# Kernel optimization log

Measured on AMD Instinct MI355X. Metric: run time of the kernel, lower is better.

Reference implementation:

```python
import jax, jax.numpy as jnp
import numpy as np

B, S, D, H = 2, 2048, 1024, 16
HD = D // H  # head_dim = 64


def setup_inputs() -> dict:
    key = jax.random.key(0)
    ks = jax.random.split(key, 6)
    scale = D ** -0.5
    x = jax.random.normal(ks[0], (B, S, D), dtype=jnp.float32)
    wq = jax.random.normal(ks[1], (D, D), dtype=jnp.float32) * scale
    wk = jax.random.normal(ks[2], (D, D), dtype=jnp.float32) * scale
    wv = jax.random.normal(ks[3], (D, D), dtype=jnp.float32) * scale
    wo = jax.random.normal(ks[4], (D, D), dtype=jnp.float32) * scale
    # RoPE frequencies: theta_i = 10000^(-2i/HD), angles[t, i] = t * theta_i
    inv_freq = 1.0 / (10000.0 ** (np.arange(0, HD, 2, dtype=np.float32) / HD))
    t = np.arange(S, dtype=np.float32)
    angles = np.outer(t, inv_freq)  # [S, HD//2]
    freqs_cos = jnp.asarray(np.cos(angles), dtype=jnp.float32)
    freqs_sin = jnp.asarray(np.sin(angles), dtype=jnp.float32)
    # additive causal mask [1,1,S,S]
    neg = jnp.float32(-1e9)
    mask = jnp.triu(jnp.full((S, S), neg, dtype=jnp.float32), k=1)[None, None]
    return {"x": x, "wq": wq, "wk": wk, "wv": wv, "wo": wo,
            "freqs_cos": freqs_cos, "freqs_sin": freqs_sin,
            "mask": mask, "start_pos": 0}


def _apply_rope(q, freqs_cos, freqs_sin):
    # q: [B, S, H, HD] -> pairs (even, odd) rotated by angle per position
    b, s, h, hd = q.shape
    q2 = q.reshape(b, s, h, hd // 2, 2)
    qr, qi = q2[..., 0], q2[..., 1]
    c = freqs_cos[None, :, None, :]  # [1, S, 1, HD//2]
    sn = freqs_sin[None, :, None, :]
    out_r = qr * c - qi * sn
    out_i = qr * sn + qi * c
    return jnp.stack([out_r, out_i], axis=-1).reshape(b, s, h, hd)


def reference(x, wq, wk, wv, wo, freqs_cos, freqs_sin, mask, start_pos):
    b, s, _ = x.shape
    xq = (x @ wq).reshape(b, s, H, HD)
    xk = (x @ wk).reshape(b, s, H, HD)
    xv = (x @ wv).reshape(b, s, H, HD)
    xq = _apply_rope(xq, freqs_cos, freqs_sin)
    xk = _apply_rope(xk, freqs_cos, freqs_sin)
    # [B, H, S, HD]
    q = xq.transpose(0, 2, 1, 3)
    k = xk.transpose(0, 2, 1, 3)
    v = xv.transpose(0, 2, 1, 3)
    scores = jnp.einsum('bhqd,bhkd->bhqk', q, k) / jnp.sqrt(jnp.float32(HD))
    scores = scores + mask
    probs = jax.nn.softmax(scores.astype(jnp.float32), axis=-1).astype(q.dtype)
    out = jnp.einsum('bhqk,bhkd->bhqd', probs, v)
    out = out.transpose(0, 2, 1, 3).reshape(b, s, H * HD)
    return out @ wo
```

## Files before the change

### kernel.cpp

```cpp
#include <hip/hip_runtime.h>

typedef unsigned short u16;
typedef __bf16 bf16x8 __attribute__((ext_vector_type(8)));
typedef float f32x4 __attribute__((ext_vector_type(4)));

#define DD 1024
#define SS 2048
#define HH 16
#define HDIM 64

#define VMCNT(N) asm volatile("s_waitcnt vmcnt(" #N ")" ::: "memory")
#define LGKMCNT0 asm volatile("s_waitcnt lgkmcnt(0)" ::: "memory")
#define MEMFENCE asm volatile("" ::: "memory")
#define SBAR __builtin_amdgcn_s_barrier()

__device__ __forceinline__ u16 f2bf(float f) {
  union { float f; unsigned u; } x; x.f = f;
  unsigned r = x.u + 0x7FFFu + ((x.u >> 16) & 1u);
  return (u16)(r >> 16);
}

__device__ __forceinline__ u16 f2bf_s(float f) {
  unsigned r;
  asm("v_cvt_pk_bf16_f32 %0, %1, %2" : "=v"(r) : "v"(f), "v"(0.f));
  return (u16)r;
}

__device__ __forceinline__ void gload_lds16(const u16* g, u16* l) {
  __builtin_amdgcn_global_load_lds((const __attribute__((address_space(1))) void*)g,
                                   (__attribute__((address_space(3))) void*)l, 16, 0, 0);
}

__global__ __launch_bounds__(256) void prep(const float* __restrict__ x,
                                            const float* __restrict__ w0, const float* __restrict__ w1,
                                            const float* __restrict__ w2, const float* __restrict__ w3,
                                            u16* __restrict__ xb, u16* __restrict__ wT) {
  __shared__ float t[32][33];
  const int id = blockIdx.x;
  const int tid = threadIdx.x;
  if (id < 4096) {
    int i = (id * 256 + tid) * 4;
    float4 v = *(const float4*)(x + i);
    union { u16 u[4]; short4 s4; } pk;
    pk.u[0] = f2bf(v.x);
    pk.u[1] = f2bf(v.y);
    pk.u[2] = f2bf(v.z);
    pk.u[3] = f2bf(v.w);
    *(short4*)(xb + i) = pk.s4;
    return;
  }
  const int tt = id - 4096;
  const int z = tt >> 10;
  const int xy = tt & 1023;
  const int j0 = (xy & 31) * 32;
  const int i0 = (xy >> 5) * 32;
  const float* w = (z == 0) ? w0 : (z == 1) ? w1 : (z == 2) ? w2 : w3;
  u16* o = wT + (size_t)z * DD * DD;
  const int tx = tid & 31, ty = tid >> 5;
#pragma unroll
  for (int r = ty; r < 32; r += 8)
    t[r][tx] = w[(size_t)(i0 + r) * DD + j0 + tx];
  __syncthreads();
#pragma unroll
  for (int r = ty; r < 32; r += 8)
    o[(size_t)(j0 + r) * DD + i0 + tx] = f2bf(t[tx][r]);
}

__global__ __launch_bounds__(512, 4) void gemm_qkv(const u16* __restrict__ xb, const u16* __restrict__ wT,
                                                   const float* __restrict__ fc, const float* __restrict__ fs,
                                                   u16* __restrict__ Qr, u16* __restrict__ Kr, u16* __restrict__ Vt) {
  __shared__ u16 As[2][128 * 64];
  __shared__ u16 Bs[2][192 * 64];
  const int tid = threadIdx.x;
  const int lane = tid & 63, wid = tid >> 6;
  const int wm = wid >> 2, wn = wid & 3;
  const int lr = lane & 15, lg = lane >> 4;
  const int id = blockIdx.x;
  const int wg = (id & 7) * 64 + (id >> 3);
  const int m0 = (wg & 31) * 128, n0 = (wg >> 5) * 192;

  f32x4 acc[4][3];
#pragma unroll
  for (int i = 0; i < 4; ++i)
#pragma unroll
    for (int j = 0; j < 3; ++j) acc[i][j] = (f32x4){0.f, 0.f, 0.f, 0.f};

  auto stage = [&](int buf, int k0) {
#pragma unroll
    for (int i = 0; i < 2; ++i) {
      int c = tid + i * 512;
      int row = c >> 3, j = (c & 7) ^ (row & 7);
      gload_lds16(xb + (size_t)(m0 + row) * DD + k0 + j * 8, &As[buf][c * 8]);
    }
#pragma unroll
    for (int i = 0; i < 3; ++i) {
      int c = tid + i * 512;
      int row = c >> 3, j = (c & 7) ^ (row & 7);
      gload_lds16(wT + (size_t)(n0 + row) * DD + k0 + j * 8, &Bs[buf][c * 8]);
    }
  };

  stage(0, 0);
  for (int kt = 0; kt < 16; ++kt) {
    const int cur = kt & 1;
    LGKMCNT0; SBAR;
    if (kt < 15) {
      stage(cur ^ 1, (kt + 1) * 64);
      VMCNT(5);
    } else {
      VMCNT(0);
    }
    SBAR; MEMFENCE;
#pragma unroll
    for (int ks = 0; ks < 2; ++ks) {
      bf16x8 af[4], bfr[3];
#pragma unroll
      for (int mi = 0; mi < 4; ++mi) {
        int row = wm * 64 + mi * 16 + lr;
        int ch = (ks * 4 + lg) ^ (row & 7);
        af[mi] = *(const bf16x8*)(&As[cur][row * 64 + ch * 8]);
      }
#pragma unroll
      for (int ni = 0; ni < 3; ++ni) {
        int row = wn * 48 + ni * 16 + lr;
        int ch = (ks * 4 + lg) ^ (row & 7);
        bfr[ni] = *(const bf16x8*)(&Bs[cur][row * 64 + ch * 8]);
      }
      __builtin_amdgcn_s_setprio(1);
#pragma unroll
      for (int mi = 0; mi < 4; ++mi)
#pragma unroll
        for (int ni = 0; ni < 3; ++ni)
          acc[mi][ni] = __builtin_amdgcn_mfma_f32_16x16x32_bf16(af[mi], bfr[ni], acc[mi][ni], 0, 0, 0);
      __builtin_amdgcn_s_setprio(0);
    }
  }

#pragma unroll
  for (int mi = 0; mi < 4; ++mi)
#pragma unroll
    for (int ni = 0; ni < 3; ++ni) {
      const int nb = n0 + wn * 48 + ni * 16;
      const int z = nb >> 10;
      const int nn = (nb & 1023) + lr;
      const int h = nn >> 6, hd = nn & 63;
      const int mb = m0 + wm * 64 + mi * 16 + lg * 4;
      const int b = mb >> 11, s = mb & 2047;
      if (z == 2) {
        union { u16 u[4]; short4 v4; } pk;
#pragma unroll
        for (int j = 0; j < 4; ++j) pk.u[j] = f2bf(acc[mi][ni][j]);
        *(short4*)(Vt + ((size_t)(b * HH + h) * HDIM + hd) * SS + s) = pk.v4;
      } else {
        u16* dst = (z == 0) ? Qr : Kr;
#pragma unroll
        for (int j = 0; j < 4; ++j) {
          float v = acc[mi][ni][j];
          float pv = __shfl_xor(v, 1);
          int fi = (s + j) * 32 + (hd >> 1);
          float c = fc[fi], sn = fs[fi];
          float o = ((hd & 1) == 0) ? (v * c - pv * sn) : (pv * sn + v * c);
          dst[((size_t)(b * HH + h) * SS + s + j) * HDIM + hd] = f2bf(o);
        }
      }
    }
}

__device__ __forceinline__ void stage_tile(const u16* __restrict__ Kh, const u16* __restrict__ Vh,
                                           int i2, u16* Kbuf, u16* Vbuf, int tid) {
#pragma unroll
  for (int k = 0; k < 2; ++k) {
    const int c = tid + k * 512;
    const int tt = c >> 9, cl = c & 511;
    const int row = cl >> 3, j = (cl & 7) ^ (row & 7);
    gload_lds16(Kh + (size_t)(i2 * 128 + tt * 64 + row) * HDIM + j * 8, Kbuf + c * 8);
    gload_lds16(Vh + (size_t)row * SS + i2 * 128 + tt * 64 + j * 8, Vbuf + c * 8);
  }
}

__device__ __forceinline__ void attn_pass(int qt, int bh, const u16* __restrict__ Qh,
                                          const u16* __restrict__ Kh, const u16* __restrict__ Vh,
                                          u16* __restrict__ Ob, u16* KbR, u16* VbR, u16* Pw,
                                          int gid, int wq) {
  const int tid = threadIdx.x;
  const int lane = tid & 63;
  const int lr = lane & 15, lg = lane >> 4;
  const int q0 = qt * 64 + wq * 16;

  bf16x8 aq[2];
#pragma unroll
  for (int ks = 0; ks < 2; ++ks)
    aq[ks] = *(const bf16x8*)(Qh + (q0 + lr) * HDIM + ks * 32 + lg * 8);

  bf16x8 ones;
  {
    union { u16 u[8]; bf16x8 v; } ou;
#pragma unroll
    for (int i = 0; i < 8; ++i) ou.u[i] = 0x3F80;
    ones = ou.v;
  }

  f32x4 o[4];
#pragma unroll
  for (int d = 0; d < 4; ++d) o[d] = (f32x4){0.f, 0.f, 0.f, 0.f};
  f32x4 ls = (f32x4){0.f, 0.f, 0.f, 0.f};

  const int n2 = (qt + 2) >> 1;

  __syncthreads();
  stage_tile(Kh, Vh, 0, KbR, VbR, tid);

  for (int i = 0; i < n2; ++i) {
    const int cur = i & 1;
    LGKMCNT0; SBAR;
    if (i + 1 < n2) {
      stage_tile(Kh, Vh, i + 1, KbR + (cur ^ 1) * 8192, VbR + (cur ^ 1) * 8192, tid);
      VMCNT(4);
    } else {
      VMCNT(0);
    }
    SBAR; MEMFENCE;

    const int t = 2 * i + gid;
    const u16* Kt = KbR + cur * 8192 + gid * 4096;
    const u16* Vtl = VbR + cur * 8192 + gid * 4096;

    f32x4 sc[4];
#pragma unroll
    for (int kb = 0; kb < 4; ++kb) sc[kb] = (f32x4){0.f, 0.f, 0.f, 0.f};
    __builtin_amdgcn_s_setprio(1);
#pragma unroll
    for (int ks = 0; ks < 2; ++ks)
#pragma unroll
      for (int kb = 0; kb < 4; ++kb) {
        int row = kb * 16 + lr;
        int ch = (ks * 4 + lg) ^ (row & 7);
        bf16x8 bk = *(const bf16x8*)(Kt + row * 64 + ch * 8);
        sc[kb] = __builtin_amdgcn_mfma_f32_16x16x32_bf16(aq[ks], bk, sc[kb], 0, 0, 0);
      }
    __builtin_amdgcn_s_setprio(0);

    if (t >= qt) {
#pragma unroll
      for (int kb = 0; kb < 4; ++kb)
#pragma unroll
        for (int j = 0; j < 4; ++j) {
          int q = q0 + lg * 4 + j;
          int kk = t * 64 + kb * 16 + lr;
          float e = __expf(sc[kb][j] * 0.125f);
          sc[kb][j] = (kk > q) ? 0.f : e;
        }
    } else {
#pragma unroll
      for (int kb = 0; kb < 4; ++kb)
#pragma unroll
        for (int j = 0; j < 4; ++j)
          sc[kb][j] = __expf(sc[kb][j] * 0.125f);
    }

#pragma unroll
    for (int kb = 0; kb < 4; ++kb)
#pragma unroll
      for (int j = 0; j < 4; ++j) {
        int rr = lg * 4 + j;
        int ccol = kb * 16 + lr;
        int ch = (ccol >> 3) ^ (rr & 7);
        Pw[rr * 64 + ch * 8 + (ccol & 7)] = f2bf_s(sc[kb][j]);
      }
#pragma unroll
    for (int ks = 0; ks < 2; ++ks) {
      int chp = (ks * 4 + lg) ^ (lr & 7);
      bf16x8 ap = *(const bf16x8*)(Pw + lr * 64 + chp * 8);
      __builtin_amdgcn_s_setprio(1);
      ls = __builtin_amdgcn_mfma_f32_16x16x32_bf16(ap, ones, ls, 0, 0, 0);
#pragma unroll
      for (int d = 0; d < 4; ++d) {
        int row = d * 16 + lr;
        int ch = (ks * 4 + lg) ^ (row & 7);
        bf16x8 bv = *(const bf16x8*)(Vtl + row * 64 + ch * 8);
        o[d] = __builtin_amdgcn_mfma_f32_16x16x32_bf16(ap, bv, o[d], 0, 0, 0);
      }
      __builtin_amdgcn_s_setprio(0);
    }
  }

  __syncthreads();
  float* mo = (float*)KbR;
  float* ml = (float*)VbR;
  if (gid == 1) {
#pragma unroll
    for (int d = 0; d < 4; ++d)
#pragma unroll
      for (int j = 0; j < 4; ++j)
        mo[(wq * 16 + lg * 4 + j) * 64 + d * 16 + lr] = o[d][j];
    if (lr == 0) {
#pragma unroll
      for (int j = 0; j < 4; ++j) ml[wq * 16 + lg * 4 + j] = ls[j];
    }
  }
  __syncthreads();
  if (gid == 0) {
    const int b = bh >> 4, h = bh & 15;
#pragma unroll
    for (int d = 0; d < 4; ++d)
#pragma unroll
      for (int j = 0; j < 4; ++j) {
        float val = o[d][j] + mo[(wq * 16 + lg * 4 + j) * 64 + d * 16 + lr];
        float lss = ls[j] + ml[wq * 16 + lg * 4 + j];
        int s = q0 + lg * 4 + j;
        int col = h * HDIM + d * 16 + lr;
        Ob[((size_t)b * SS + s) * DD + col] = f2bf(val / lss);
      }
  }
}

__global__ __launch_bounds__(512, 4) void attn(const u16* __restrict__ Qr, const u16* __restrict__ Kr,
                                               const u16* __restrict__ Vt, u16* __restrict__ Ob) {
  __shared__ u16 Kb[2][2][64 * 64];
  __shared__ u16 Vb[2][2][64 * 64];
  __shared__ u16 Ps[8][16 * 64];
  const int id = blockIdx.x;
  const int xcd = id & 7;
  const int r = id >> 3;
  const int pair = r & 15;
  const int bh = xcd * 4 + (r >> 4);
  const u16* Qh = Qr + (size_t)bh * SS * HDIM;
  const u16* Kh = Kr + (size_t)bh * SS * HDIM;
  const u16* Vh = Vt + (size_t)bh * HDIM * SS;
  const int wid = threadIdx.x >> 6;
  const int gid = wid >> 2, wq = wid & 3;
  u16* Pw = &Ps[wid][0];
  attn_pass(pair, bh, Qh, Kh, Vh, Ob, &Kb[0][0][0], &Vb[0][0][0], Pw, gid, wq);
  attn_pass(31 - pair, bh, Qh, Kh, Vh, Ob, &Kb[0][0][0], &Vb[0][0][0], Pw, gid, wq);
}

__global__ __launch_bounds__(512, 4) void gemm_wo(const u16* __restrict__ Ab, const u16* __restrict__ woT,
                                                  float* __restrict__ out) {
  __shared__ u16 As[2][128 * 64];
  __shared__ u16 Bs[2][128 * 64];
  const int tid = threadIdx.x;
  const int lane = tid & 63, wid = tid >> 6;
  const int wm = wid >> 1, wn = wid & 1;
  const int lr = lane & 15, lg = lane >> 4;
  const int id = blockIdx.x;
  const int wg = (id & 7) * 32 + (id >> 3);
  const int m0 = (wg & 31) * 128, n0 = (wg >> 5) * 128;

  f32x4 acc[2][4];
#pragma unroll
  for (int i = 0; i < 2; ++i)
#pragma unroll
    for (int j = 0; j < 4; ++j) acc[i][j] = (f32x4){0.f, 0.f, 0.f, 0.f};

  auto stage = [&](int buf, int k0) {
#pragma unroll
    for (int i = 0; i < 2; ++i) {
      int c = tid + i * 512;
      int row = c >> 3, j = (c & 7) ^ (row & 7);
      gload_lds16(Ab + (size_t)(m0 + row) * DD + k0 + j * 8, &As[buf][c * 8]);
      gload_lds16(woT + (size_t)(n0 + row) * DD + k0 + j * 8, &Bs[buf][c * 8]);
    }
  };

  stage(0, 0);
  for (int kt = 0; kt < 16; ++kt) {
    const int cur = kt & 1;
    LGKMCNT0; SBAR;
    if (kt < 15) {
      stage(cur ^ 1, (kt + 1) * 64);
      VMCNT(4);
    } else {
      VMCNT(0);
    }
    SBAR; MEMFENCE;
#pragma unroll
    for (int ks = 0; ks < 2; ++ks) {
      bf16x8 af[2], bfr[4];
#pragma unroll
      for (int mi = 0; mi < 2; ++mi) {
        int row = wm * 32 + mi * 16 + lr;
        int ch = (ks * 4 + lg) ^ (row & 7);
        af[mi] = *(const bf16x8*)(&As[cur][row * 64 + ch * 8]);
      }
#pragma unroll
      for (int ni = 0; ni < 4; ++ni) {
        int row = wn * 64 + ni * 16 + lr;
        int ch = (ks * 4 + lg) ^ (row & 7);
        bfr[ni] = *(const bf16x8*)(&Bs[cur][row * 64 + ch * 8]);
      }
      __builtin_amdgcn_s_setprio(1);
#pragma unroll
      for (int mi = 0; mi < 2; ++mi)
#pragma unroll
        for (int ni = 0; ni < 4; ++ni)
          acc[mi][ni] = __builtin_amdgcn_mfma_f32_16x16x32_bf16(af[mi], bfr[ni], acc[mi][ni], 0, 0, 0);
      __builtin_amdgcn_s_setprio(0);
    }
  }

#pragma unroll
  for (int mi = 0; mi < 2; ++mi)
#pragma unroll
    for (int ni = 0; ni < 4; ++ni)
#pragma unroll
      for (int j = 0; j < 4; ++j) {
        int m = m0 + wm * 32 + mi * 16 + lg * 4 + j;
        int n = n0 + wn * 64 + ni * 16 + lr;
        out[(size_t)m * DD + n] = acc[mi][ni][j];
      }
}

extern "C" void kernel_launch(void* const* d_in, const int* in_sizes, int n_in,
                              void* d_out, int out_size, void* d_ws, size_t ws_size,
                              hipStream_t stream) {
  const float* x  = (const float*)d_in[0];
  const float* wq = (const float*)d_in[1];
  const float* wk = (const float*)d_in[2];
  const float* wv = (const float*)d_in[3];
  const float* wo = (const float*)d_in[4];
  const float* fc = (const float*)d_in[5];
  const float* fs = (const float*)d_in[6];
  float* out = (float*)d_out;

  char* ws = (char*)d_ws;
  u16* xb = (u16*)(ws);
  u16* wT = (u16*)(ws + (8ull << 20));
  u16* Qr = (u16*)(ws + (16ull << 20));
  u16* Kr = (u16*)(ws + (24ull << 20));
  u16* Vt = (u16*)(ws + (32ull << 20));
  u16* Ob = (u16*)(ws + (40ull << 20));

  prep<<<8192, 256, 0, stream>>>(x, wq, wk, wv, wo, xb, wT);
  gemm_qkv<<<512, 512, 0, stream>>>(xb, wT, fc, fs, Qr, Kr, Vt);
  attn<<<512, 512, 0, stream>>>(Qr, Kr, Vt, Ob);
  gemm_wo<<<256, 512, 0, stream>>>(Ob, wT + 3ull * DD * DD, out);
}
```

Before: 103.9 us.

## Restructure attention into one query tile per block with direct V loads

The attention kernel now launches 1024 blocks of 256 threads. Each block handles a single 64-row query tile, with tiles ordered heaviest first, instead of pairing tiles and splitting keys across two wave groups. Only K is staged in LDS; V is read straight from global memory in the PV step, which removes the cross-group reduction through shared memory. The softmax scale and log2(e) are folded into Q in the QKV epilogue so the inner loop can use exp2f. The trade-off is that uncoalesced V reads from global/L2 replace LDS reuse, and load balancing now depends on block scheduling.

```diff
diff --git a/kernel.cpp b/kernel.cpp
--- a/kernel.cpp
+++ b/kernel.cpp
@@ -8,6 +8,7 @@
 #define SS 2048
 #define HH 16
 #define HDIM 64
+#define QSCALE 0.1803368801111204f
 
 #define VMCNT(N) asm volatile("s_waitcnt vmcnt(" #N ")" ::: "memory")
 #define LGKMCNT0 asm volatile("s_waitcnt lgkmcnt(0)" ::: "memory")
@@ -160,32 +161,36 @@
           int fi = (s + j) * 32 + (hd >> 1);
           float c = fc[fi], sn = fs[fi];
           float o = ((hd & 1) == 0) ? (v * c - pv * sn) : (pv * sn + v * c);
+          if (z == 0) o *= QSCALE;
           dst[((size_t)(b * HH + h) * SS + s + j) * HDIM + hd] = f2bf(o);
         }
       }
     }
 }
 
-__device__ __forceinline__ void stage_tile(const u16* __restrict__ Kh, const u16* __restrict__ Vh,
-                                           int i2, u16* Kbuf, u16* Vbuf, int tid) {
-#pragma unroll
-  for (int k = 0; k < 2; ++k) {
-    const int c = tid + k * 512;
-    const int tt = c >> 9, cl = c & 511;
-    const int row = cl >> 3, j = (cl & 7) ^ (row & 7);
-    gload_lds16(Kh + (size_t)(i2 * 128 + tt * 64 + row) * HDIM + j * 8, Kbuf + c * 8);
-    gload_lds16(Vh + (size_t)row * SS + i2 * 128 + tt * 64 + j * 8, Vbuf + c * 8);
-  }
-}
-
-__device__ __forceinline__ void attn_pass(int qt, int bh, const u16* __restrict__ Qh,
-                                          const u16* __restrict__ Kh, const u16* __restrict__ Vh,
-                                          u16* __restrict__ Ob, u16* KbR, u16* VbR, u16* Pw,
-                                          int gid, int wq) {
+__global__ __launch_bounds__(256, 6) void attn(const u16* __restrict__ Qr, const u16* __restrict__ Kr,
+                                               const u16* __restrict__ Vt, u16* __restrict__ Ob) {
+  __shared__ u16 Kb[2][64 * 64];
+  __shared__ u16 Ps[4][16 * 64];
+  const int id = blockIdx.x;
+  const int xcd = id & 7;
+  const int r = id >> 3;
+  const int qt = 31 - (r >> 2);
+  const int bh = xcd * 4 + (r & 3);
+
+  const u16* Qh = Qr + (size_t)bh * SS * HDIM;
+  const u16* Kh = Kr + (size_t)bh * SS * HDIM;
+  const u16* Vh = Vt + (size_t)bh * HDIM * SS;
+
   const int tid = threadIdx.x;
-  const int lane = tid & 63;
+  const int lane = tid & 63, wid = tid >> 6;
   const int lr = lane & 15, lg = lane >> 4;
-  const int q0 = qt * 64 + wq * 16;
+  const int q0 = qt * 64 + wid * 16;
+  u16* Pw = &Ps[wid][0];
+
+  const int c0 = tid, c1 = tid + 256;
+  const int srow0 = c0 >> 3, sj0 = (c0 & 7) ^ (srow0 & 7);
+  const int srow1 = c1 >> 3, sj1 = (c1 & 7) ^ (srow1 & 7);
 
   bf16x8 aq[2];
 #pragma unroll
@@ -205,26 +210,22 @@
   for (int d = 0; d < 4; ++d) o[d] = (f32x4){0.f, 0.f, 0.f, 0.f};
   f32x4 ls = (f32x4){0.f, 0.f, 0.f, 0.f};
 
-  const int n2 = (qt + 2) >> 1;
-
-  __syncthreads();
-  stage_tile(Kh, Vh, 0, KbR, VbR, tid);
-
-  for (int i = 0; i < n2; ++i) {
-    const int cur = i & 1;
+  gload_lds16(Kh + (size_t)srow0 * HDIM + sj0 * 8, &Kb[0][c0 * 8]);
+  gload_lds16(Kh + (size_t)srow1 * HDIM + sj1 * 8, &Kb[0][c1 * 8]);
+
+  for (int t = 0; t <= qt; ++t) {
+    const int cur = t & 1;
     LGKMCNT0; SBAR;
-    if (i + 1 < n2) {
-      stage_tile(Kh, Vh, i + 1, KbR + (cur ^ 1) * 8192, VbR + (cur ^ 1) * 8192, tid);
-      VMCNT(4);
+    if (t < qt) {
+      const int g0 = (t + 1) * 64;
+      gload_lds16(Kh + (size_t)(g0 + srow0) * HDIM + sj0 * 8, &Kb[cur ^ 1][c0 * 8]);
+      gload_lds16(Kh + (size_t)(g0 + srow1) * HDIM + sj1 * 8, &Kb[cur ^ 1][c1 * 8]);
+      VMCNT(2);
     } else {
       VMCNT(0);
     }
     SBAR; MEMFENCE;
 
-    const int t = 2 * i + gid;
-    const u16* Kt = KbR + cur * 8192 + gid * 4096;
-    const u16* Vtl = VbR + cur * 8192 + gid * 4096;
-
     f32x4 sc[4];
 #pragma unroll
     for (int kb = 0; kb < 4; ++kb) sc[kb] = (f32x4){0.f, 0.f, 0.f, 0.f};
@@ -235,19 +236,19 @@
       for (int kb = 0; kb < 4; ++kb) {
         int row = kb * 16 + lr;
         int ch = (ks * 4 + lg) ^ (row & 7);
-        bf16x8 bk = *(const bf16x8*)(Kt + row * 64 + ch * 8);
+        bf16x8 bk = *(const bf16x8*)(&Kb[cur][row * 64 + ch * 8]);
         sc[kb] = __builtin_amdgcn_mfma_f32_16x16x32_bf16(aq[ks], bk, sc[kb], 0, 0, 0);
       }
     __builtin_amdgcn_s_setprio(0);
 
-    if (t >= qt) {
+    if (t == qt) {
 #pragma unroll
       for (int kb = 0; kb < 4; ++kb)
 #pragma unroll
         for (int j = 0; j < 4; ++j) {
           int q = q0 + lg * 4 + j;
           int kk = t * 64 + kb * 16 + lr;
-          float e = __expf(sc[kb][j] * 0.125f);
+          float e = exp2f(sc[kb][j]);
           sc[kb][j] = (kk > q) ? 0.f : e;
         }
     } else {
@@ -255,7 +256,7 @@
       for (int kb = 0; kb < 4; ++kb)
 #pragma unroll
         for (int j = 0; j < 4; ++j)
-          sc[kb][j] = __expf(sc[kb][j] * 0.125f);
+          sc[kb][j] = exp2f(sc[kb][j]);
     }
 
 #pragma unroll
@@ -271,67 +272,24 @@
     for (int ks = 0; ks < 2; ++ks) {
       int chp = (ks * 4 + lg) ^ (lr & 7);
       bf16x8 ap = *(const bf16x8*)(Pw + lr * 64 + chp * 8);
-      __builtin_amdgcn_s_setprio(1);
       ls = __builtin_amdgcn_mfma_f32_16x16x32_bf16(ap, ones, ls, 0, 0, 0);
 #pragma unroll
       for (int d = 0; d < 4; ++d) {
-        int row = d * 16 + lr;
-        int ch = (ks * 4 + lg) ^ (row & 7);
-        bf16x8 bv = *(const bf16x8*)(Vtl + row * 64 + ch * 8);
+        bf16x8 bv = *(const bf16x8*)(Vh + (size_t)(d * 16 + lr) * SS + t * 64 + ks * 32 + lg * 8);
         o[d] = __builtin_amdgcn_mfma_f32_16x16x32_bf16(ap, bv, o[d], 0, 0, 0);
       }
-      __builtin_amdgcn_s_setprio(0);
-    }
-  }
-
-  __syncthreads();
-  float* mo = (float*)KbR;
-  float* ml = (float*)VbR;
-  if (gid == 1) {
-#pragma unroll
-    for (int d = 0; d < 4; ++d)
-#pragma unroll
-      for (int j = 0; j < 4; ++j)
-        mo[(wq * 16 + lg * 4 + j) * 64 + d * 16 + lr] = o[d][j];
-    if (lr == 0) {
-#pragma unroll
-      for (int j = 0; j < 4; ++j) ml[wq * 16 + lg * 4 + j] = ls[j];
-    }
-  }
-  __syncthreads();
-  if (gid == 0) {
-    const int b = bh >> 4, h = bh & 15;
-#pragma unroll
-    for (int d = 0; d < 4; ++d)
-#pragma unroll
-      for (int j = 0; j < 4; ++j) {
-        float val = o[d][j] + mo[(wq * 16 + lg * 4 + j) * 64 + d * 16 + lr];
-        float lss = ls[j] + ml[wq * 16 + lg * 4 + j];
-        int s = q0 + lg * 4 + j;
-        int col = h * HDIM + d * 16 + lr;
-        Ob[((size_t)b * SS + s) * DD + col] = f2bf(val / lss);
-      }
-  }
-}
-
-__global__ __launch_bounds__(512, 4) void attn(const u16* __restrict__ Qr, const u16* __restrict__ Kr,
-                                               const u16* __restrict__ Vt, u16* __restrict__ Ob) {
-  __shared__ u16 Kb[2][2][64 * 64];
-  __shared__ u16 Vb[2][2][64 * 64];
-  __shared__ u16 Ps[8][16 * 64];
-  const int id = blockIdx.x;
-  const int xcd = id & 7;
-  const int r = id >> 3;
-  const int pair = r & 15;
-  const int bh = xcd * 4 + (r >> 4);
-  const u16* Qh = Qr + (size_t)bh * SS * HDIM;
-  const u16* Kh = Kr + (size_t)bh * SS * HDIM;
-  const u16* Vh = Vt + (size_t)bh * HDIM * SS;
-  const int wid = threadIdx.x >> 6;
-  const int gid = wid >> 2, wq = wid & 3;
-  u16* Pw = &Ps[wid][0];
-  attn_pass(pair, bh, Qh, Kh, Vh, Ob, &Kb[0][0][0], &Vb[0][0][0], Pw, gid, wq);
-  attn_pass(31 - pair, bh, Qh, Kh, Vh, Ob, &Kb[0][0][0], &Vb[0][0][0], Pw, gid, wq);
+    }
+  }
+
+  const int b = bh >> 4, h = bh & 15;
+#pragma unroll
+  for (int d = 0; d < 4; ++d)
+#pragma unroll
+    for (int j = 0; j < 4; ++j) {
+      int s = q0 + lg * 4 + j;
+      int col = h * HDIM + d * 16 + lr;
+      Ob[((size_t)b * SS + s) * DD + col] = f2bf(o[d][j] / ls[j]);
+    }
 }
 
 __global__ __launch_bounds__(512, 4) void gemm_wo(const u16* __restrict__ Ab, const u16* __restrict__ woT,
@@ -432,6 +390,6 @@
 
   prep<<<8192, 256, 0, stream>>>(x, wq, wk, wv, wo, xb, wT);
   gemm_qkv<<<512, 512, 0, stream>>>(xb, wT, fc, fs, Qr, Kr, Vt);
-  attn<<<512, 512, 0, stream>>>(Qr, Kr, Vt, Ob);
+  attn<<<1024, 256, 0, stream>>>(Qr, Kr, Vt, Ob);
   gemm_wo<<<256, 512, 0, stream>>>(Ob, wT + 3ull * DD * DD, out);
 }
```

Result: slower. 179.3 us (+72.6%).
